# Kernel optimization log

Hardware: AMD Instinct MI355X
Metric: run time of the kernel (lower is better)

Reference implementation:

```python
import jax, jax.numpy as jnp
import numpy as np

N, E = 50000, 800000
NF, EF, S = 128, 64, 128

def _lin(key, fan_in, fan_out):
    k1, k2 = jax.random.split(key)
    lim = 1.0 / np.sqrt(fan_in)
    W = jax.random.uniform(k1, (fan_in, fan_out), jnp.float32, -lim, lim)
    b = jax.random.uniform(k2, (fan_out,), jnp.float32, -lim, lim)
    return W, b

def setup_inputs() -> dict:
    key = jax.random.key(0)
    ks = jax.random.split(key, 12)
    x = jax.random.normal(ks[0], (N, NF), jnp.float32)
    edge_index = jax.random.randint(ks[1], (2, E), 0, N, jnp.int64)
    edge_attr = jax.random.normal(ks[2], (E, EF), jnp.float32)
    Wn, bn = _lin(ks[3], NF, S)
    We, be = _lin(ks[4], EF, S)
    Wzc, bzc = _lin(ks[5], S, S)   # GCNConv weight/bias (z gate)
    Wzl, bzl = _lin(ks[6], 2 * S, S)
    Wrc, brc = _lin(ks[7], S, S)
    Wrl, brl = _lin(ks[8], 2 * S, S)
    Whc, bhc = _lin(ks[9], S, S)
    Whl, bhl = _lin(ks[10], 2 * S, S)
    Wout, bout = _lin(ks[11], 3 * S, 1)
    return dict(x=x, edge_index=edge_index, edge_attr=edge_attr,
                Wn=Wn, bn=bn, We=We, be=be,
                Wzc=Wzc, bzc=bzc, Wzl=Wzl, bzl=bzl,
                Wrc=Wrc, brc=brc, Wrl=Wrl, brl=brl,
                Whc=Whc, bhc=bhc, Whl=Whl, bhl=bhl,
                Wout=Wout, bout=bout)

def reference(x, edge_index, edge_attr, Wn, bn, We, be,
              Wzc, bzc, Wzl, bzl, Wrc, brc, Wrl, brl,
              Whc, bhc, Whl, bhl, Wout, bout):
    n = x.shape[0]
    src, dst = edge_index[0], edge_index[1]
    xe = jax.nn.relu(x @ Wn + bn)                      # [N,S]
    ea = jax.nn.relu(edge_attr @ We + be)              # [E,S]
    # GCNConv normalization with self-loops (shared across the 3 gates)
    loop = jnp.arange(n)
    s2 = jnp.concatenate([src, loop])
    d2 = jnp.concatenate([dst, loop])
    deg = jax.ops.segment_sum(jnp.ones(s2.shape[0], xe.dtype), d2, n)
    dinv = jax.lax.rsqrt(deg)                          # deg >= 1 (self loops)
    norm = (dinv[s2] * dinv[d2])[:, None]              # [E+N,1]
    def gcn(W, b):
        xw = xe @ W
        return jax.ops.segment_sum(xw[s2] * norm, d2, n) + b
    H = jnp.zeros_like(xe)
    Z = jax.nn.sigmoid(jnp.concatenate([gcn(Wzc, bzc), H], 1) @ Wzl + bzl)
    R = jax.nn.sigmoid(jnp.concatenate([gcn(Wrc, brc), H], 1) @ Wrl + brl)
    Ht = jnp.tanh(jnp.concatenate([gcn(Whc, bhc), H * R], 1) @ Whl + bhl)
    H = Z * H + (1.0 - Z) * Ht                          # [N,S]
    edge_h = jnp.concatenate([H[src], H[dst], ea], axis=1)  # [E,3S]
    return edge_h @ Wout + bout                         # [E,1]
```

## Files before the change

### kernel.cpp

```cpp
#include <hip/hip_runtime.h>
#include <hip/hip_bf16.h>
#include <math.h>

#define NN 50000
#define EE 800000

typedef __bf16 bf16x8 __attribute__((ext_vector_type(8)));
typedef float f32x4 __attribute__((ext_vector_type(4)));
typedef unsigned int u32x4 __attribute__((ext_vector_type(4)));

__global__ void k_deg_wprep(const int* __restrict__ ei, int* __restrict__ deg,
                            const float* __restrict__ Wzc, const float* __restrict__ bzc,
                            const float* __restrict__ Wzl, const float* __restrict__ bzl,
                            const float* __restrict__ Whc, const float* __restrict__ bhc,
                            const float* __restrict__ Whl, const float* __restrict__ bhl,
                            float* __restrict__ Wcat, float* __restrict__ cb) {
    if (blockIdx.x < 128) {
        int i = blockIdx.x;
        int k = threadIdx.x;
        if (k < 128) {
            float sz = 0.f, sh = 0.f;
            for (int j = 0; j < 128; j++) {
                sz += Wzc[i * 128 + j] * Wzl[j * 128 + k];
                sh += Whc[i * 128 + j] * Whl[j * 128 + k];
            }
            Wcat[i * 256 + 2 * k]     = sz;
            Wcat[i * 256 + 2 * k + 1] = sh;
            if (i == 0) {
                float bz = bzl[k], bh = bhl[k];
                for (int j = 0; j < 128; j++) {
                    bz += bzc[j] * Wzl[j * 128 + k];
                    bh += bhc[j] * Whl[j * 128 + k];
                }
                cb[2 * k]     = bz;
                cb[2 * k + 1] = bh;
            }
        }
    } else {
        int e = (blockIdx.x - 128) * 256 + threadIdx.x;
        if (e < EE) atomicAdd(&deg[ei[EE + e]], 1);
    }
}

__global__ __launch_bounds__(256) void k_g1_mfma(const float* __restrict__ x,
                                                 const float* __restrict__ Wn,
                                                 const float* __restrict__ bn,
                                                 const int* __restrict__ deg,
                                                 __hip_bfloat16* __restrict__ xs) {
    const int lane = threadIdx.x & 63;
    const int ln = lane & 15;
    const int q  = lane >> 4;
    const int wid = (blockIdx.x * 256 + threadIdx.x) >> 6;
    const int nw  = gridDim.x * 4;
    const int ch  = wid & 1;
    const int step = nw >> 1;

    bf16x8 bfrag[4][4];
#pragma unroll
    for (int t = 0; t < 4; t++)
#pragma unroll
        for (int kc = 0; kc < 4; kc++)
#pragma unroll
            for (int j = 0; j < 8; j++)
                bfrag[t][kc][j] = (__bf16)Wn[(kc * 32 + q * 8 + j) * 128 + ch * 64 + t * 16 + ln];
    float biasR[4];
#pragma unroll
    for (int t = 0; t < 4; t++) biasR[t] = bn[ch * 64 + t * 16 + ln];

    for (int rt = wid >> 1; rt < 3125; rt += step) {
        const int e0 = rt * 16;
        const float* arow = x + (size_t)(e0 + ln) * 128;
        bf16x8 af[4];
#pragma unroll
        for (int kc = 0; kc < 4; kc++) {
            float4 v0 = *(const float4*)(arow + kc * 32 + q * 8);
            float4 v1 = *(const float4*)(arow + kc * 32 + q * 8 + 4);
            af[kc][0] = (__bf16)v0.x; af[kc][1] = (__bf16)v0.y;
            af[kc][2] = (__bf16)v0.z; af[kc][3] = (__bf16)v0.w;
            af[kc][4] = (__bf16)v1.x; af[kc][5] = (__bf16)v1.y;
            af[kc][6] = (__bf16)v1.z; af[kc][7] = (__bf16)v1.w;
        }
        f32x4 acc[4];
#pragma unroll
        for (int t = 0; t < 4; t++) acc[t] = (f32x4){0.f, 0.f, 0.f, 0.f};
#pragma unroll
        for (int t = 0; t < 4; t++)
#pragma unroll
            for (int kc = 0; kc < 4; kc++)
                acc[t] = __builtin_amdgcn_mfma_f32_16x16x32_bf16(af[kc], bfrag[t][kc], acc[t], 0, 0, 0);

        float diR[4];
#pragma unroll
        for (int r = 0; r < 4; r++) diR[r] = rsqrtf((float)(deg[e0 + q * 4 + r] + 1));
#pragma unroll
        for (int t = 0; t < 4; t++)
#pragma unroll
            for (int r = 0; r < 4; r++) {
                float v = fmaxf(acc[t][r] + biasR[t], 0.f) * diR[r];
                xs[(size_t)(e0 + q * 4 + r) * 128 + ch * 64 + t * 16 + ln] = __float2bfloat16(v);
            }
    }
}

__global__ __launch_bounds__(256) void k_gate_mfma(const unsigned int* __restrict__ aggu,
                                                   const float* __restrict__ Wcat,
                                                   const float* __restrict__ cb,
                                                   const float* __restrict__ Wout,
                                                   float* __restrict__ aArr,
                                                   float* __restrict__ bArr) {
    const int lane = threadIdx.x & 63;
    const int ln = lane & 15;
    const int q  = lane >> 4;
    const int wid = (blockIdx.x * 256 + threadIdx.x) >> 6;
    const int nw  = gridDim.x * 4;
    const int cq  = wid & 3;
    const int step = nw >> 2;

    bf16x8 bfrag[4][4];
#pragma unroll
    for (int t = 0; t < 4; t++)
#pragma unroll
        for (int kc = 0; kc < 4; kc++)
#pragma unroll
            for (int j = 0; j < 8; j++)
                bfrag[t][kc][j] = (__bf16)Wcat[(kc * 32 + q * 8 + j) * 256 + cq * 64 + t * 16 + ln];

    float cbR[4], wAR[4], wBR[4];
#pragma unroll
    for (int t = 0; t < 4; t++) {
        int col = cq * 64 + t * 16 + ln;
        cbR[t] = cb[col];
        int k = col >> 1;
        wAR[t] = Wout[k];
        wBR[t] = Wout[128 + k];
    }
    const bool odd = (ln & 1);

    for (int rt = wid >> 2; rt < 3125; rt += step) {
        const int e0 = rt * 16;
        const u32x4* arow = (const u32x4*)aggu + (size_t)(e0 + ln) * 16;
        bf16x8 af[4];
#pragma unroll
        for (int kc = 0; kc < 4; kc++) {
            u32x4 uv = arow[kc * 4 + q];
            af[kc] = __builtin_bit_cast(bf16x8, uv);
        }
        f32x4 acc[4];
#pragma unroll
        for (int t = 0; t < 4; t++) acc[t] = (f32x4){0.f, 0.f, 0.f, 0.f};
#pragma unroll
        for (int t = 0; t < 4; t++)
#pragma unroll
            for (int kc = 0; kc < 4; kc++)
                acc[t] = __builtin_amdgcn_mfma_f32_16x16x32_bf16(af[kc], bfrag[t][kc], acc[t], 0, 0, 0);

        float pa[4] = {0.f, 0.f, 0.f, 0.f};
        float pb[4] = {0.f, 0.f, 0.f, 0.f};
#pragma unroll
        for (int t = 0; t < 4; t++)
#pragma unroll
            for (int r = 0; r < 4; r++) {
                float val = acc[t][r] + cbR[t];
                float s = odd ? tanhf(val) : (1.f / (1.f + expf(-val)));
                float partner = __shfl_xor(s, 1);
                if (!odd) {
                    float h = (1.f - s) * partner;
                    pa[r] += h * wAR[t];
                    pb[r] += h * wBR[t];
                }
            }
#pragma unroll
        for (int off = 1; off < 16; off <<= 1) {
#pragma unroll
            for (int r = 0; r < 4; r++) {
                pa[r] += __shfl_xor(pa[r], off);
                pb[r] += __shfl_xor(pb[r], off);
            }
        }
        if (ln < 4) {
            float v = (ln == 0) ? pa[0] : (ln == 1) ? pa[1] : (ln == 2) ? pa[2] : pa[3];
            atomicAdd(&aArr[e0 + q * 4 + ln], v);
        } else if (ln < 8) {
            int r = ln - 4;
            float v = (r == 0) ? pb[0] : (r == 1) ? pb[1] : (r == 2) ? pb[2] : pb[3];
            atomicAdd(&bArr[e0 + q * 4 + r], v);
        }
    }
}

__global__ void k_scan_a(const int* __restrict__ deg, int* __restrict__ partial) {
    __shared__ int s[256];
    int i = blockIdx.x * 256 + threadIdx.x;
    s[threadIdx.x] = (i < NN) ? deg[i] : 0;
    __syncthreads();
    for (int off = 128; off > 0; off >>= 1) {
        if (threadIdx.x < off) s[threadIdx.x] += s[threadIdx.x + off];
        __syncthreads();
    }
    if (threadIdx.x == 0) partial[blockIdx.x] = s[0];
}

__global__ void k_scan_c(const int* __restrict__ deg, const int* __restrict__ partial,
                         int* __restrict__ rowptr, int* __restrict__ cursor) {
    __shared__ int s[256];
    __shared__ int ps[256];
    int i = blockIdx.x * 256 + threadIdx.x;
    int v = (i < NN) ? deg[i] : 0;
    s[threadIdx.x] = v;
    ps[threadIdx.x] = (threadIdx.x < blockIdx.x) ? partial[threadIdx.x] : 0;
    __syncthreads();
    for (int off = 128; off > 0; off >>= 1) {
        if (threadIdx.x < off) ps[threadIdx.x] += ps[threadIdx.x + off];
        __syncthreads();
    }
    for (int off = 1; off < 256; off <<= 1) {
        int t = (threadIdx.x >= off) ? s[threadIdx.x - off] : 0;
        __syncthreads();
        s[threadIdx.x] += t;
        __syncthreads();
    }
    int excl = s[threadIdx.x] - v + ps[0];
    if (i < NN) { rowptr[i] = excl; cursor[i] = excl; }
    if (i == 0) rowptr[NN] = EE;
}

__global__ void k_fill(const int* __restrict__ ei, int* __restrict__ cursor,
                       int* __restrict__ col) {
    int e = blockIdx.x * 256 + threadIdx.x;
    if (e < EE) {
        int d = ei[EE + e];
        int p = atomicAdd(&cursor[d], 1);
        col[p] = ei[e];
    }
}

__global__ __launch_bounds__(256) void k_gather(const unsigned int* __restrict__ xsu,
                                                const int* __restrict__ rowptr,
                                                const int* __restrict__ col,
                                                const int* __restrict__ deg,
                                                unsigned int* __restrict__ aggu) {
    int gt = blockIdx.x * 256 + threadIdx.x;
    int node = gt >> 6;
    int lane = threadIdx.x & 63;
    if (node >= NN) return;
    int beg = rowptr[node], end = rowptr[node + 1];
    unsigned int u = xsu[(size_t)node * 64 + lane];
    float a0 = __uint_as_float(u << 16);
    float a1 = __uint_as_float(u & 0xFFFF0000u);
    int p = beg;
    while (p < end) {
        int rem = end - p;
        int chunk = rem < 64 ? rem : 64;
        int cv = (lane < chunk) ? col[p + lane] : 0;
        int j = 0;
        for (; j + 8 <= chunk; j += 8) {
            int s0 = __shfl(cv, j + 0);
            int s1 = __shfl(cv, j + 1);
            int s2 = __shfl(cv, j + 2);
            int s3 = __shfl(cv, j + 3);
            int s4 = __shfl(cv, j + 4);
            int s5 = __shfl(cv, j + 5);
            int s6 = __shfl(cv, j + 6);
            int s7 = __shfl(cv, j + 7);
            unsigned int u0 = xsu[(size_t)s0 * 64 + lane];
            unsigned int u1 = xsu[(size_t)s1 * 64 + lane];
            unsigned int u2 = xsu[(size_t)s2 * 64 + lane];
            unsigned int u3 = xsu[(size_t)s3 * 64 + lane];
            unsigned int u4 = xsu[(size_t)s4 * 64 + lane];
            unsigned int u5 = xsu[(size_t)s5 * 64 + lane];
            unsigned int u6 = xsu[(size_t)s6 * 64 + lane];
            unsigned int u7 = xsu[(size_t)s7 * 64 + lane];
            a0 += __uint_as_float(u0 << 16) + __uint_as_float(u1 << 16)
                + __uint_as_float(u2 << 16) + __uint_as_float(u3 << 16)
                + __uint_as_float(u4 << 16) + __uint_as_float(u5 << 16)
                + __uint_as_float(u6 << 16) + __uint_as_float(u7 << 16);
            a1 += __uint_as_float(u0 & 0xFFFF0000u) + __uint_as_float(u1 & 0xFFFF0000u)
                + __uint_as_float(u2 & 0xFFFF0000u) + __uint_as_float(u3 & 0xFFFF0000u)
                + __uint_as_float(u4 & 0xFFFF0000u) + __uint_as_float(u5 & 0xFFFF0000u)
                + __uint_as_float(u6 & 0xFFFF0000u) + __uint_as_float(u7 & 0xFFFF0000u);
        }
        for (; j < chunk; j++) {
            int s = __shfl(cv, j);
            unsigned int uv = xsu[(size_t)s * 64 + lane];
            a0 += __uint_as_float(uv << 16);
            a1 += __uint_as_float(uv & 0xFFFF0000u);
        }
        p += 64;
    }
    float di = rsqrtf((float)(deg[node] + 1));
    __hip_bfloat16 b0 = __float2bfloat16(a0 * di);
    __hip_bfloat16 b1 = __float2bfloat16(a1 * di);
    unsigned int lo = *(unsigned short*)&b0;
    unsigned int hi = *(unsigned short*)&b1;
    aggu[(size_t)node * 64 + lane] = lo | (hi << 16);
}

__global__ __launch_bounds__(256) void k_edge_mfma(const float* __restrict__ EA,
                                                   const int* __restrict__ ei,
                                                   const float* __restrict__ We,
                                                   const float* __restrict__ be,
                                                   const float* __restrict__ Wout,
                                                   const float* __restrict__ boutp,
                                                   const float* __restrict__ aArr,
                                                   const float* __restrict__ bArr,
                                                   float* __restrict__ out) {
    const int lane = threadIdx.x & 63;
    const int ln = lane & 15;
    const int q  = lane >> 4;
    const int wid = (blockIdx.x * 256 + threadIdx.x) >> 6;
    const int nw  = gridDim.x * 4;

    bf16x8 bfrag[2][8];
#pragma unroll
    for (int h = 0; h < 2; h++)
#pragma unroll
        for (int t = 0; t < 8; t++)
#pragma unroll
            for (int j = 0; j < 8; j++)
                bfrag[h][t][j] = (__bf16)We[(h * 32 + q * 8 + j) * 128 + t * 16 + ln];

    float beR[8], w3R[8];
#pragma unroll
    for (int t = 0; t < 8; t++) {
        beR[t] = be[t * 16 + ln];
        w3R[t] = Wout[256 + t * 16 + ln];
    }
    const float b0 = boutp[0];

    for (int tile = wid; tile < EE / 16; tile += nw) {
        const int e0 = tile * 16;
        const float* arow = EA + (size_t)(e0 + ln) * 64;
        float4 v0 = *(const float4*)(arow + q * 8);
        float4 v1 = *(const float4*)(arow + q * 8 + 4);
        float4 v2 = *(const float4*)(arow + 32 + q * 8);
        float4 v3 = *(const float4*)(arow + 32 + q * 8 + 4);
        bf16x8 af0, af1;
        af0[0] = (__bf16)v0.x; af0[1] = (__bf16)v0.y; af0[2] = (__bf16)v0.z; af0[3] = (__bf16)v0.w;
        af0[4] = (__bf16)v1.x; af0[5] = (__bf16)v1.y; af0[6] = (__bf16)v1.z; af0[7] = (__bf16)v1.w;
        af1[0] = (__bf16)v2.x; af1[1] = (__bf16)v2.y; af1[2] = (__bf16)v2.z; af1[3] = (__bf16)v2.w;
        af1[4] = (__bf16)v3.x; af1[5] = (__bf16)v3.y; af1[6] = (__bf16)v3.z; af1[7] = (__bf16)v3.w;

        f32x4 acc[8];
#pragma unroll
        for (int t = 0; t < 8; t++) acc[t] = (f32x4){0.f, 0.f, 0.f, 0.f};
#pragma unroll
        for (int t = 0; t < 8; t++)
            acc[t] = __builtin_amdgcn_mfma_f32_16x16x32_bf16(af0, bfrag[0][t], acc[t], 0, 0, 0);
#pragma unroll
        for (int t = 0; t < 8; t++)
            acc[t] = __builtin_amdgcn_mfma_f32_16x16x32_bf16(af1, bfrag[1][t], acc[t], 0, 0, 0);

        float part[4] = {0.f, 0.f, 0.f, 0.f};
#pragma unroll
        for (int t = 0; t < 8; t++)
#pragma unroll
            for (int r = 0; r < 4; r++) {
                float y = acc[t][r] + beR[t];
                y = fmaxf(y, 0.f);
                part[r] += y * w3R[t];
            }
#pragma unroll
        for (int off = 1; off < 16; off <<= 1) {
#pragma unroll
            for (int r = 0; r < 4; r++) part[r] += __shfl_xor(part[r], off);
        }
        if (ln < 4) {
            float c = (ln == 0) ? part[0] : (ln == 1) ? part[1] : (ln == 2) ? part[2] : part[3];
            int e = e0 + q * 4 + ln;
            out[e] = c + aArr[ei[e]] + bArr[ei[EE + e]] + b0;
        }
    }
}

extern "C" void kernel_launch(void* const* d_in, const int* in_sizes, int n_in,
                              void* d_out, int out_size, void* d_ws, size_t ws_size,
                              hipStream_t stream) {
    const float* x    = (const float*)d_in[0];
    const int*   ei   = (const int*)d_in[1];
    const float* ea   = (const float*)d_in[2];
    const float* Wn   = (const float*)d_in[3];
    const float* bn   = (const float*)d_in[4];
    const float* We   = (const float*)d_in[5];
    const float* be   = (const float*)d_in[6];
    const float* Wzc  = (const float*)d_in[7];
    const float* bzc  = (const float*)d_in[8];
    const float* Wzl  = (const float*)d_in[9];
    const float* bzl  = (const float*)d_in[10];
    const float* Whc  = (const float*)d_in[15];
    const float* bhc  = (const float*)d_in[16];
    const float* Whl  = (const float*)d_in[17];
    const float* bhl  = (const float*)d_in[18];
    const float* Wout = (const float*)d_in[19];
    const float* bout = (const float*)d_in[20];
    float* out = (float*)d_out;

    char* w = (char*)d_ws;
    auto carve = [&](size_t bytes) {
        void* p = (void*)w;
        w += (bytes + 255) / 256 * 256;
        return p;
    };
    int*   deg     = (int*)carve((size_t)NN * 4);
    float* aArr    = (float*)carve((size_t)NN * 4);
    float* bArr    = (float*)carve((size_t)NN * 4);
    size_t zbytes  = (size_t)((char*)(bArr + NN) - (char*)deg);
    __hip_bfloat16* xs = (__hip_bfloat16*)carve((size_t)NN * 128 * 2);
    unsigned int* aggu = (unsigned int*)carve((size_t)NN * 64 * 4);
    float* Wcat    = (float*)carve(128 * 256 * 4);
    float* cb      = (float*)carve(256 * 4);
    int*   rowptr  = (int*)carve((size_t)(NN + 1) * 4);
    int*   cursor  = (int*)carve((size_t)NN * 4);
    int*   col     = (int*)carve((size_t)EE * 4);
    int*   partial = (int*)carve(256 * 4);

    hipMemsetAsync(deg, 0, zbytes, stream);

    k_deg_wprep<<<128 + 3125, 256, 0, stream>>>(ei, deg, Wzc, bzc, Wzl, bzl,
                                                Whc, bhc, Whl, bhl, Wcat, cb);

    k_g1_mfma<<<384, 256, 0, stream>>>(x, Wn, bn, deg, xs);

    const int NB = (NN + 255) / 256;
    k_scan_a<<<NB, 256, 0, stream>>>(deg, partial);
    k_scan_c<<<NB, 256, 0, stream>>>(deg, partial, rowptr, cursor);
    k_fill<<<3125, 256, 0, stream>>>(ei, cursor, col);

    k_gather<<<(NN * 64 + 255) / 256, 256, 0, stream>>>((const unsigned int*)xs, rowptr, col, deg, aggu);

    k_gate_mfma<<<512, 256, 0, stream>>>(aggu, Wcat, cb, Wout, aArr, bArr);

    k_edge_mfma<<<2048, 256, 0, stream>>>(ea, ei, We, be, Wout, bout, aArr, bArr, out);
}
```

Before: 522.7 us.

## Drop gate atomics via block reduction, fuse scan kernels, simplify gather loop

The gate kernel now assigns one 16-row tile per block, with its four waves covering the four column quarters. Partial sums are reduced through shared memory and written with plain stores instead of global atomicAdd. The two scan kernels become one single-pass scan that publishes block totals with release stores and spin-waits on earlier blocks, removing one launch. The gather loop is rewritten as a fixed unrolled 8-wide loop with clamped column indices and predicated accumulation, and the memset range now covers the partial array instead of aArr/bArr. The spin-wait depends on earlier blocks being scheduled first, and the gather may issue some redundant loads in the tail.

```diff
diff --git a/kernel.cpp b/kernel.cpp
--- a/kernel.cpp
+++ b/kernel.cpp
@@ -108,13 +108,12 @@
                                                    const float* __restrict__ Wout,
                                                    float* __restrict__ aArr,
                                                    float* __restrict__ bArr) {
-    const int lane = threadIdx.x & 63;
+    __shared__ float red[4][32];
+    const int tid = threadIdx.x;
+    const int lane = tid & 63;
     const int ln = lane & 15;
     const int q  = lane >> 4;
-    const int wid = (blockIdx.x * 256 + threadIdx.x) >> 6;
-    const int nw  = gridDim.x * 4;
-    const int cq  = wid & 3;
-    const int step = nw >> 2;
+    const int w  = tid >> 6;
 
     bf16x8 bfrag[4][4];
 #pragma unroll
@@ -123,12 +122,12 @@
         for (int kc = 0; kc < 4; kc++)
 #pragma unroll
             for (int j = 0; j < 8; j++)
-                bfrag[t][kc][j] = (__bf16)Wcat[(kc * 32 + q * 8 + j) * 256 + cq * 64 + t * 16 + ln];
+                bfrag[t][kc][j] = (__bf16)Wcat[(kc * 32 + q * 8 + j) * 256 + w * 64 + t * 16 + ln];
 
     float cbR[4], wAR[4], wBR[4];
 #pragma unroll
     for (int t = 0; t < 4; t++) {
-        int col = cq * 64 + t * 16 + ln;
+        int col = w * 64 + t * 16 + ln;
         cbR[t] = cb[col];
         int k = col >> 1;
         wAR[t] = Wout[k];
@@ -136,7 +135,7 @@
     }
     const bool odd = (ln & 1);
 
-    for (int rt = wid >> 2; rt < 3125; rt += step) {
+    for (int rt = blockIdx.x; rt < 3125; rt += gridDim.x) {
         const int e0 = rt * 16;
         const u32x4* arow = (const u32x4*)aggu + (size_t)(e0 + ln) * 16;
         bf16x8 af[4];
@@ -177,46 +176,52 @@
                 pb[r] += __shfl_xor(pb[r], off);
             }
         }
-        if (ln < 4) {
-            float v = (ln == 0) ? pa[0] : (ln == 1) ? pa[1] : (ln == 2) ? pa[2] : pa[3];
-            atomicAdd(&aArr[e0 + q * 4 + ln], v);
-        } else if (ln < 8) {
-            int r = ln - 4;
-            float v = (r == 0) ? pb[0] : (r == 1) ? pb[1] : (r == 2) ? pb[2] : pb[3];
-            atomicAdd(&bArr[e0 + q * 4 + r], v);
-        }
-    }
-}
-
-__global__ void k_scan_a(const int* __restrict__ deg, int* __restrict__ partial) {
-    __shared__ int s[256];
-    int i = blockIdx.x * 256 + threadIdx.x;
-    s[threadIdx.x] = (i < NN) ? deg[i] : 0;
-    __syncthreads();
-    for (int off = 128; off > 0; off >>= 1) {
-        if (threadIdx.x < off) s[threadIdx.x] += s[threadIdx.x + off];
         __syncthreads();
-    }
-    if (threadIdx.x == 0) partial[blockIdx.x] = s[0];
-}
-
-__global__ void k_scan_c(const int* __restrict__ deg, const int* __restrict__ partial,
-                         int* __restrict__ rowptr, int* __restrict__ cursor) {
+        if (ln == 0) {
+#pragma unroll
+            for (int r = 0; r < 4; r++) {
+                red[w][q * 4 + r]      = pa[r];
+                red[w][16 + q * 4 + r] = pb[r];
+            }
+        }
+        __syncthreads();
+        if (tid < 32) {
+            float sum = red[0][tid] + red[1][tid] + red[2][tid] + red[3][tid];
+            if (tid < 16) aArr[e0 + tid] = sum;
+            else          bArr[e0 + tid - 16] = sum;
+        }
+    }
+}
+
+__global__ void k_scan(const int* __restrict__ deg, int* __restrict__ partial,
+                       int* __restrict__ rowptr, int* __restrict__ cursor) {
     __shared__ int s[256];
     __shared__ int ps[256];
-    int i = blockIdx.x * 256 + threadIdx.x;
+    const int b = blockIdx.x;
+    const int i = b * 256 + threadIdx.x;
     int v = (i < NN) ? deg[i] : 0;
     s[threadIdx.x] = v;
-    ps[threadIdx.x] = (threadIdx.x < blockIdx.x) ? partial[threadIdx.x] : 0;
     __syncthreads();
-    for (int off = 128; off > 0; off >>= 1) {
-        if (threadIdx.x < off) ps[threadIdx.x] += ps[threadIdx.x + off];
-        __syncthreads();
-    }
     for (int off = 1; off < 256; off <<= 1) {
         int t = (threadIdx.x >= off) ? s[threadIdx.x - off] : 0;
         __syncthreads();
         s[threadIdx.x] += t;
+        __syncthreads();
+    }
+    if (threadIdx.x == 255)
+        __hip_atomic_store(&partial[b], s[255] + 1, __ATOMIC_RELEASE, __HIP_MEMORY_SCOPE_AGENT);
+    int contrib = 0;
+    if (threadIdx.x < b) {
+        int pv;
+        do {
+            pv = __hip_atomic_load(&partial[threadIdx.x], __ATOMIC_ACQUIRE, __HIP_MEMORY_SCOPE_AGENT);
+        } while (pv == 0);
+        contrib = pv - 1;
+    }
+    ps[threadIdx.x] = contrib;
+    __syncthreads();
+    for (int off = 128; off > 0; off >>= 1) {
+        if (threadIdx.x < off) ps[threadIdx.x] += ps[threadIdx.x + off];
         __syncthreads();
     }
     int excl = s[threadIdx.x] - v + ps[0];
@@ -247,45 +252,22 @@
     unsigned int u = xsu[(size_t)node * 64 + lane];
     float a0 = __uint_as_float(u << 16);
     float a1 = __uint_as_float(u & 0xFFFF0000u);
-    int p = beg;
-    while (p < end) {
-        int rem = end - p;
-        int chunk = rem < 64 ? rem : 64;
-        int cv = (lane < chunk) ? col[p + lane] : 0;
-        int j = 0;
-        for (; j + 8 <= chunk; j += 8) {
-            int s0 = __shfl(cv, j + 0);
-            int s1 = __shfl(cv, j + 1);
-            int s2 = __shfl(cv, j + 2);
-            int s3 = __shfl(cv, j + 3);
-            int s4 = __shfl(cv, j + 4);
-            int s5 = __shfl(cv, j + 5);
-            int s6 = __shfl(cv, j + 6);
-            int s7 = __shfl(cv, j + 7);
-            unsigned int u0 = xsu[(size_t)s0 * 64 + lane];
-            unsigned int u1 = xsu[(size_t)s1 * 64 + lane];
-            unsigned int u2 = xsu[(size_t)s2 * 64 + lane];
-            unsigned int u3 = xsu[(size_t)s3 * 64 + lane];
-            unsigned int u4 = xsu[(size_t)s4 * 64 + lane];
-            unsigned int u5 = xsu[(size_t)s5 * 64 + lane];
-            unsigned int u6 = xsu[(size_t)s6 * 64 + lane];
-            unsigned int u7 = xsu[(size_t)s7 * 64 + lane];
-            a0 += __uint_as_float(u0 << 16) + __uint_as_float(u1 << 16)
-                + __uint_as_float(u2 << 16) + __uint_as_float(u3 << 16)
-                + __uint_as_float(u4 << 16) + __uint_as_float(u5 << 16)
-                + __uint_as_float(u6 << 16) + __uint_as_float(u7 << 16);
-            a1 += __uint_as_float(u0 & 0xFFFF0000u) + __uint_as_float(u1 & 0xFFFF0000u)
-                + __uint_as_float(u2 & 0xFFFF0000u) + __uint_as_float(u3 & 0xFFFF0000u)
-                + __uint_as_float(u4 & 0xFFFF0000u) + __uint_as_float(u5 & 0xFFFF0000u)
-                + __uint_as_float(u6 & 0xFFFF0000u) + __uint_as_float(u7 & 0xFFFF0000u);
-        }
-        for (; j < chunk; j++) {
-            int s = __shfl(cv, j);
-            unsigned int uv = xsu[(size_t)s * 64 + lane];
-            a0 += __uint_as_float(uv << 16);
-            a1 += __uint_as_float(uv & 0xFFFF0000u);
-        }
-        p += 64;
+    for (int p = beg; p < end; p += 64) {
+        int navail = end - p;
+        int clamp = (lane < navail) ? lane : (navail - 1);
+        int cv = col[p + clamp];
+        int chunk = navail < 64 ? navail : 64;
+        for (int j = 0; j < chunk; j += 8) {
+#pragma unroll
+            for (int jj = 0; jj < 8; jj++) {
+                int s = __shfl(cv, j + jj);
+                unsigned int uv = xsu[(size_t)s * 64 + lane];
+                if (j + jj < chunk) {
+                    a0 += __uint_as_float(uv << 16);
+                    a1 += __uint_as_float(uv & 0xFFFF0000u);
+                }
+            }
+        }
     }
     float di = rsqrtf((float)(deg[node] + 1));
     __hip_bfloat16 b0 = __float2bfloat16(a0 * di);
@@ -401,9 +383,10 @@
         return p;
     };
     int*   deg     = (int*)carve((size_t)NN * 4);
+    int*   partial = (int*)carve(256 * 4);
+    size_t zbytes  = (size_t)((char*)(partial + 256) - (char*)deg);
     float* aArr    = (float*)carve((size_t)NN * 4);
     float* bArr    = (float*)carve((size_t)NN * 4);
-    size_t zbytes  = (size_t)((char*)(bArr + NN) - (char*)deg);
     __hip_bfloat16* xs = (__hip_bfloat16*)carve((size_t)NN * 128 * 2);
     unsigned int* aggu = (unsigned int*)carve((size_t)NN * 64 * 4);
     float* Wcat    = (float*)carve(128 * 256 * 4);
@@ -411,7 +394,6 @@
     int*   rowptr  = (int*)carve((size_t)(NN + 1) * 4);
     int*   cursor  = (int*)carve((size_t)NN * 4);
     int*   col     = (int*)carve((size_t)EE * 4);
-    int*   partial = (int*)carve(256 * 4);
 
     hipMemsetAsync(deg, 0, zbytes, stream);
 
@@ -421,8 +403,7 @@
     k_g1_mfma<<<384, 256, 0, stream>>>(x, Wn, bn, deg, xs);
 
     const int NB = (NN + 255) / 256;
-    k_scan_a<<<NB, 256, 0, stream>>>(deg, partial);
-    k_scan_c<<<NB, 256, 0, stream>>>(deg, partial, rowptr, cursor);
+    k_scan<<<NB, 256, 0, stream>>>(deg, partial, rowptr, cursor);
     k_fill<<<3125, 256, 0, stream>>>(ei, cursor, col);
 
     k_gather<<<(NN * 64 + 255) / 256, 256, 0, stream>>>((const unsigned int*)xs, rowptr, col, deg, aggu);
```

New measurement: 558.7 us. 1.07x slower.
